# Performance work log

Hardware: AMD Instinct MI355X
Metric: run time of the kernel (lower is better)

Reference implementation:

```python
import jax, jax.numpy as jnp
import numpy as np
from jax import lax

CLIP = 1.0  # STE clip value for both input and kernel quantizers
EPS = 1e-3  # keras BatchNormalization default epsilon

@jax.custom_vjp
def binarize(x):
    # sign with >=0 -> +1, <0 -> -1 (matches tf.where(x>=0, 1, -1))
    return jnp.where(x >= 0, jnp.ones_like(x), -jnp.ones_like(x))

def _bin_fwd(x):
    return binarize(x), x

def _bin_bwd(x, g):
    # straight-through estimator: pass grad where |x| <= clip, else 0
    return (jnp.where(jnp.abs(x) <= CLIP, g, jnp.zeros_like(g)),)

binarize.defvjp(_bin_fwd, _bin_bwd)

def setup_inputs() -> dict:
    key = jax.random.key(0)
    k1, k2, k3 = jax.random.split(key, 3)
    B, H, Wd, C = 32, 56, 56, 128
    x = jax.random.normal(k1, (B, H, Wd, C), dtype=jnp.float32)
    W = jax.random.normal(k2, (3, 3, C, C), dtype=jnp.float32) * 0.05  # HWIO
    gamma = jnp.ones((C,), dtype=jnp.float32) + 0.1 * jax.random.normal(k3, (C,), dtype=jnp.float32)
    beta = jnp.zeros((C,), dtype=jnp.float32)
    return {"x": x, "W": W, "gamma": gamma, "beta": beta}

def reference(x, W, gamma, beta):
    # binarize activations and weights (sign with STE grad)
    xb = binarize(x)
    wb = binarize(W)
    # 3x3 SAME conv, stride 1, NHWC / HWIO
    y = lax.conv_general_dilated(
        xb, wb, window_strides=(1, 1), padding='SAME',
        dimension_numbers=('NHWC', 'HWIO', 'NHWC'))
    r = jax.nn.relu(y)
    # training-mode batch norm over axes (0,1,2)
    mean = jnp.mean(r, axis=(0, 1, 2), keepdims=True)
    var = jnp.var(r, axis=(0, 1, 2), keepdims=True)
    r_std = (r - mean) * lax.rsqrt(var + EPS)
    out_bn = gamma * r_std + beta
    # shortcut add with (un-binarized) input
    return out_bn + x
```

## Files before the change

kernel.cpp:

```cpp
#include <hip/hip_runtime.h>

#define CH    128
#define HH    56
#define WW    56
#define BB    32
#define NPIX  (BB * HH * WW)
#define NSLOT 16

#define XROW   7424
#define XBATCH 430592
#define LDSROW 8448
#define SWZ(pl, ci) ((ci) ^ (((pl) & 7) << 4))

typedef int i32x4  __attribute__((ext_vector_type(4)));
typedef int i32x16 __attribute__((ext_vector_type(16)));

__device__ __forceinline__ void mfma_i8(i32x16& acc, i32x4 a, i32x4 b) {
    asm("v_mfma_i32_32x32x32_i8 %0, %1, %2, %0" : "+v"(acc) : "v"(a), "v"(b));
}

__global__ __launch_bounds__(256) void prep_k(const float* __restrict__ x,
                                              const float* __restrict__ Wt,
                                              signed char* __restrict__ xi8,
                                              signed char* __restrict__ wfrag,
                                              unsigned long long* __restrict__ accum) {
    int bx = blockIdx.x, tid = threadIdx.x;
    if (bx < 12544) {
        int t = bx * 256 + tid;
        int p = t >> 5;
        int ci0 = (t & 31) * 4;
        int w = p % WW;
        int t2 = p / WW;
        int h = t2 % HH;
        int b = t2 / HH;
        float4 v = ((const float4*)x)[t];
        unsigned o = (v.x >= 0.f ? 0x01u : 0xFFu)
                   | ((v.y >= 0.f ? 0x01u : 0xFFu) << 8)
                   | ((v.z >= 0.f ? 0x01u : 0xFFu) << 16)
                   | ((v.w >= 0.f ? 0x01u : 0xFFu) << 24);
        *(unsigned*)(xi8 + (size_t)b * XBATCH + (size_t)(h + 1) * XROW + (w + 1) * 128 + ci0) = o;
    } else if (bx < 12772) {
        int c = (bx - 12544) * 256 + tid;
        int cell = c >> 3, q = c & 7;
        int b = cell / 228, e = cell % 228;
        int row, col;
        if (e < 58)       { row = 0;       col = e; }
        else if (e < 116) { row = 57;      col = e - 58; }
        else if (e < 172) { row = e - 115; col = 0; }
        else              { row = e - 171; col = 57; }
        i32x4 z = {0, 0, 0, 0};
        *(i32x4*)(xi8 + (size_t)b * XBATCH + (size_t)row * XROW + col * 128 + q * 16) = z;
    } else if (bx < 12808) {
        int i = (bx - 12772) * 256 + tid;
        int n = i / 2304;
        int r = i % 2304;
        int q = r / 64;
        int L = r % 64;
        int tap = q >> 2, kk = q & 3;
        int co = 32 * n + (L & 31);
        int kbase = 32 * kk + (L >> 5) * 16;
        i32x4 o;
        #pragma unroll
        for (int d = 0; d < 4; ++d) {
            unsigned u = 0;
            #pragma unroll
            for (int by = 0; by < 4; ++by) {
                int ci = kbase + 4 * d + by;
                unsigned s = (Wt[((size_t)tap * 128 + ci) * 128 + co] >= 0.f) ? 0x01u : 0xFFu;
                u |= s << (8 * by);
            }
            o[d] = (int)u;
        }
        *(i32x4*)(wfrag + (size_t)i * 16) = o;
    } else {
        for (int k = tid; k < NSLOT * 256; k += 256) accum[k] = 0ull;
    }
}

__global__ __launch_bounds__(512) void gemm_k(const signed char* __restrict__ xi8,
                                              const signed char* __restrict__ wfrag,
                                              unsigned long long* __restrict__ accum,
                                              unsigned short* __restrict__ rb) {
    __shared__ alignas(16) char sm[3 * LDSROW];

    int L = threadIdx.x & 63, w = threadIdx.x >> 6;
    int n32 = w & 3, sh = w >> 2;
    int l31 = L & 31, hi = L >> 5;

    int aoff[3][4];
    #pragma unroll
    for (int dw = 0; dw < 3; ++dw) {
        int pld = l31 + dw;
        int pl = 32 * sh + pld;
        #pragma unroll
        for (int kk = 0; kk < 4; ++kk)
            aoff[dw][kk] = pl * 128 + ((32 * kk + 16 * hi) ^ ((pld & 7) << 4));
    }

    const i32x4* bfp = (const i32x4*)wfrag + (size_t)n32 * 36 * 64;
    i32x4 bfr[36];
    #pragma unroll
    for (int q = 0; q < 36; ++q) bfr[q] = bfp[q * 64 + L];

    int co = 32 * n32 + l31;

    #pragma unroll 1
    for (int t = 0; t < 7; ++t) {
        int id = blockIdx.x * 7 + t;
        int ph = 1 + (id % HH);
        int b  = id / HH;

        for (int c = threadIdx.x; c < 1392; c += 512) {
            int rr = c / 464;
            int off = (c % 464) * 16;
            int p = off >> 7, ci0 = off & 127;
            i32x4 v = *(const i32x4*)(xi8 + (size_t)b * XBATCH + (size_t)(ph - 1 + rr) * XROW + off);
            int pl = p + 1;
            *(i32x4*)(sm + rr * LDSROW + pl * 128 + SWZ(pl, ci0)) = v;
        }
        for (int c = threadIdx.x; c < 192; c += 512) {
            int rr = c / 64, g = c % 64;
            int gp = g >> 3, ci0 = (g & 7) * 16;
            int pl = (gp == 0) ? 0 : (58 + gp);
            i32x4 z = {0, 0, 0, 0};
            *(i32x4*)(sm + rr * LDSROW + pl * 128 + SWZ(pl, ci0)) = z;
        }
        __syncthreads();

        i32x16 acc = {};
        #pragma unroll
        for (int q = 0; q < 36; ++q) {
            int tap = q >> 2, kk = q & 3;
            int dh = tap / 3, dw = tap % 3;
            i32x4 a = *(const i32x4*)(sm + dh * LDSROW + aoff[dw][kk]);
            mfma_i8(acc, a, bfr[q]);
        }
        asm volatile("s_nop 7\n\ts_nop 7\n\ts_nop 7" : "+v"(acc));

        unsigned s1 = 0, s2 = 0;
        size_t rbase = (((size_t)b * HH + (ph - 1)) * WW) * CH + co;
        #pragma unroll
        for (int reg = 0; reg < 16; ++reg) {
            int pw = 32 * sh + (reg & 3) + 8 * (reg >> 2) + 4 * hi;
            int y = acc[reg];
            int r = y > 0 ? y : 0;
            if (pw >= 1 && pw <= WW) {
                s1 += (unsigned)r;
                s2 += (unsigned)__mul24(r, r);
                rb[rbase + (size_t)(pw - 1) * CH] = (unsigned short)r;
            }
        }
        s1 += __shfl_xor(s1, 32);
        s2 += __shfl_xor(s2, 32);
        if (hi == 0) {
            int slot = id & (NSLOT - 1);
            atomicAdd(&accum[slot * 256 + co],       (unsigned long long)s1);
            atomicAdd(&accum[slot * 256 + 128 + co], (unsigned long long)s2);
        }
        __syncthreads();
    }
}

__global__ __launch_bounds__(256) void out_k(const unsigned short* __restrict__ rb,
                                             const unsigned long long* __restrict__ accum,
                                             const float* __restrict__ gamma,
                                             const float* __restrict__ beta,
                                             const float* __restrict__ x,
                                             float* __restrict__ out) {
    __shared__ float2 ssl[CH];
    int tid = threadIdx.x;
    if (tid < CH) {
        unsigned long long a1 = 0, a2 = 0;
        #pragma unroll
        for (int s = 0; s < NSLOT; ++s) {
            a1 += accum[s * 256 + tid];
            a2 += accum[s * 256 + 128 + tid];
        }
        float N    = (float)NPIX;
        float mean = (float)a1 / N;
        float ex2  = (float)a2 / N;
        float var  = fmaf(-mean, mean, ex2);
        float rstd = 1.0f / sqrtf(var + 1e-3f);
        float sc   = gamma[tid] * rstd;
        float2 v;
        v.x = sc;
        v.y = fmaf(-mean, sc, beta[tid]);
        ssl[tid] = v;
    }
    __syncthreads();

    int c4 = tid & 31;
    float2 s0 = ssl[c4 * 4 + 0], s1 = ssl[c4 * 4 + 1];
    float2 s2 = ssl[c4 * 4 + 2], s3 = ssl[c4 * 4 + 3];
    int base = blockIdx.x * 2048 + tid;
    #pragma unroll
    for (int k = 0; k < 8; ++k) {
        int idx4 = base + k * 256;
        ushort4 r = ((const ushort4*)rb)[idx4];
        float4 xv = ((const float4*)x)[idx4];
        float4 o;
        o.x = fmaf((float)r.x, s0.x, s0.y + xv.x);
        o.y = fmaf((float)r.y, s1.x, s1.y + xv.y);
        o.z = fmaf((float)r.z, s2.x, s2.y + xv.z);
        o.w = fmaf((float)r.w, s3.x, s3.y + xv.w);
        ((float4*)out)[idx4] = o;
    }
}

extern "C" void kernel_launch(void* const* d_in, const int* in_sizes, int n_in,
                              void* d_out, int out_size, void* d_ws, size_t ws_size,
                              hipStream_t stream) {
    const float* x     = (const float*)d_in[0];
    const float* Wt    = (const float*)d_in[1];
    const float* gamma = (const float*)d_in[2];
    const float* beta  = (const float*)d_in[3];
    float* out = (float*)d_out;
    char* ws = (char*)d_ws;

    signed char* xi8   = (signed char*)ws;
    signed char* wfrag = (signed char*)(ws + 13778944);
    unsigned long long* accum = (unsigned long long*)(ws + 13926400);
    unsigned short* rb = (unsigned short*)(ws + 13959168);

    hipLaunchKernelGGL(prep_k, dim3(12809), dim3(256), 0, stream, x, Wt, xi8, wfrag, accum);
    hipLaunchKernelGGL(gemm_k, dim3(256), dim3(512), 0, stream, xi8, wfrag, accum, rb);
    hipLaunchKernelGGL(out_k,  dim3(NPIX * CH / 4 / 2048), dim3(256), 0, stream,
                       rb, accum, gamma, beta, x, out);
}
```

Before: 62.01 us.

## Use rolling 4-row LDS ring buffer with prefetch and split MFMA accumulators

The conv kernel now keeps a 4-slot ring of input rows in LDS. It loads the first three rows once, then each iteration prefetches only the next row into registers while computing and writes it after the epilogue. This removes the redundant reload of three rows per output row and overlaps the global load with MFMA work, at the cost of one fewer barrier-separated phase. MFMAs also alternate between two accumulators to break the dependency chain, which adds extra VGPRs and a final add.

```diff
diff --git a/kernel.cpp b/kernel.cpp
--- a/kernel.cpp
+++ b/kernel.cpp
@@ -81,20 +81,23 @@
                                               const signed char* __restrict__ wfrag,
                                               unsigned long long* __restrict__ accum,
                                               unsigned short* __restrict__ rb) {
-    __shared__ alignas(16) char sm[3 * LDSROW];
+    __shared__ alignas(16) char sm[4 * LDSROW];
+
+    int ph0 = 1 + ((blockIdx.x * 7) % HH);
+    int b   = (blockIdx.x * 7) / HH;
 
     int L = threadIdx.x & 63, w = threadIdx.x >> 6;
     int n32 = w & 3, sh = w >> 2;
     int l31 = L & 31, hi = L >> 5;
 
-    int aoff[3][4];
+    int coff[3][4];
     #pragma unroll
     for (int dw = 0; dw < 3; ++dw) {
         int pld = l31 + dw;
         int pl = 32 * sh + pld;
         #pragma unroll
         for (int kk = 0; kk < 4; ++kk)
-            aoff[dw][kk] = pl * 128 + ((32 * kk + 16 * hi) ^ ((pld & 7) << 4));
+            coff[dw][kk] = pl * 128 + ((32 * kk + 16 * hi) ^ ((pld & 7) << 4));
     }
 
     const i32x4* bfp = (const i32x4*)wfrag + (size_t)n32 * 36 * 64;
@@ -104,45 +107,61 @@
 
     int co = 32 * n32 + l31;
 
+    for (int c = threadIdx.x; c < 1392; c += 512) {
+        int rr = c / 464;
+        int off = (c % 464) * 16;
+        int row = ph0 - 1 + rr;
+        int p = off >> 7, ci0 = off & 127;
+        i32x4 v = *(const i32x4*)(xi8 + (size_t)b * XBATCH + (size_t)row * XROW + off);
+        int pl = p + 1;
+        *(i32x4*)(sm + (row & 3) * LDSROW + pl * 128 + SWZ(pl, ci0)) = v;
+    }
+    if (threadIdx.x < 256) {
+        int slot = threadIdx.x >> 6, g = threadIdx.x & 63;
+        int gp = g >> 3, ci0 = (g & 7) * 16;
+        int pl = (gp == 0) ? 0 : (58 + gp);
+        i32x4 z = {0, 0, 0, 0};
+        *(i32x4*)(sm + slot * LDSROW + pl * 128 + SWZ(pl, ci0)) = z;
+    }
+    __syncthreads();
+
     #pragma unroll 1
     for (int t = 0; t < 7; ++t) {
+        int ph = ph0 + t;
         int id = blockIdx.x * 7 + t;
-        int ph = 1 + (id % HH);
-        int b  = id / HH;
-
-        for (int c = threadIdx.x; c < 1392; c += 512) {
-            int rr = c / 464;
-            int off = (c % 464) * 16;
+
+        i32x4 stv;
+        int stdst = -1;
+        if (t < 6 && threadIdx.x < 464) {
+            int nrow = ph + 2;
+            int off = threadIdx.x * 16;
             int p = off >> 7, ci0 = off & 127;
-            i32x4 v = *(const i32x4*)(xi8 + (size_t)b * XBATCH + (size_t)(ph - 1 + rr) * XROW + off);
+            stv = *(const i32x4*)(xi8 + (size_t)b * XBATCH + (size_t)nrow * XROW + off);
             int pl = p + 1;
-            *(i32x4*)(sm + rr * LDSROW + pl * 128 + SWZ(pl, ci0)) = v;
-        }
-        for (int c = threadIdx.x; c < 192; c += 512) {
-            int rr = c / 64, g = c % 64;
-            int gp = g >> 3, ci0 = (g & 7) * 16;
-            int pl = (gp == 0) ? 0 : (58 + gp);
-            i32x4 z = {0, 0, 0, 0};
-            *(i32x4*)(sm + rr * LDSROW + pl * 128 + SWZ(pl, ci0)) = z;
-        }
-        __syncthreads();
-
-        i32x16 acc = {};
+            stdst = (nrow & 3) * LDSROW + pl * 128 + SWZ(pl, ci0);
+        }
+
+        int rs[3] = { ((ph - 1) & 3) * LDSROW, (ph & 3) * LDSROW, ((ph + 1) & 3) * LDSROW };
+
+        i32x16 acc0 = {}, acc1 = {};
         #pragma unroll
         for (int q = 0; q < 36; ++q) {
             int tap = q >> 2, kk = q & 3;
             int dh = tap / 3, dw = tap % 3;
-            i32x4 a = *(const i32x4*)(sm + dh * LDSROW + aoff[dw][kk]);
-            mfma_i8(acc, a, bfr[q]);
-        }
-        asm volatile("s_nop 7\n\ts_nop 7\n\ts_nop 7" : "+v"(acc));
+            i32x4 a = *(const i32x4*)(sm + rs[dh] + coff[dw][kk]);
+            if (q & 1) mfma_i8(acc1, a, bfr[q]);
+            else       mfma_i8(acc0, a, bfr[q]);
+        }
+        asm volatile("s_nop 7\n\ts_nop 7\n\ts_nop 7" : "+v"(acc0), "+v"(acc1));
+        #pragma unroll
+        for (int e = 0; e < 16; ++e) acc0[e] += acc1[e];
 
         unsigned s1 = 0, s2 = 0;
         size_t rbase = (((size_t)b * HH + (ph - 1)) * WW) * CH + co;
         #pragma unroll
         for (int reg = 0; reg < 16; ++reg) {
             int pw = 32 * sh + (reg & 3) + 8 * (reg >> 2) + 4 * hi;
-            int y = acc[reg];
+            int y = acc0[reg];
             int r = y > 0 ? y : 0;
             if (pw >= 1 && pw <= WW) {
                 s1 += (unsigned)r;
@@ -157,6 +176,9 @@
             atomicAdd(&accum[slot * 256 + co],       (unsigned long long)s1);
             atomicAdd(&accum[slot * 256 + 128 + co], (unsigned long long)s2);
         }
+
+        if (stdst >= 0) *(i32x4*)(sm + stdst) = stv;
+
         __syncthreads();
     }
 }
```

After: 60.43 us. -2.5%, faster.
